# Kernel optimization log

Measured on AMD Instinct MI355X. Metric: run time of the kernel, lower is better.

Reference implementation:

```python
import jax, jax.numpy as jnp
import numpy as np
import math

B, S, C, H = 32, 500, 1024, 16
D = C // H  # head dim = 64

def setup_inputs() -> dict:
    key = jax.random.key(0)
    ks = jax.random.split(key, 9)
    sc = 1.0 / math.sqrt(C)
    return {
        "x": jax.random.normal(ks[0], (B, S, C), dtype=jnp.float32),
        "Wq": jax.random.normal(ks[1], (C, C), dtype=jnp.float32) * sc,
        "bq": jnp.zeros((C,), dtype=jnp.float32),
        "Wk": jax.random.normal(ks[2], (C, C), dtype=jnp.float32) * sc,
        "bk": jnp.zeros((C,), dtype=jnp.float32),
        "Wv": jax.random.normal(ks[3], (C, C), dtype=jnp.float32) * sc,
        "bv": jnp.zeros((C,), dtype=jnp.float32),
        "Wp": jax.random.normal(ks[4], (C, C), dtype=jnp.float32) * sc,
        "bp": jnp.zeros((C,), dtype=jnp.float32),
    }

def reference(x, Wq, bq, Wk, bk, Wv, bv, Wp, bp):
    # Projections -> [B, H, S, D]
    q = (x @ Wq + bq).reshape(B, S, H, D).transpose(0, 2, 1, 3)
    k = (x @ Wk + bk).reshape(B, S, H, D).transpose(0, 2, 1, 3)
    v = (x @ Wv + bv).reshape(B, S, H, D).transpose(0, 2, 1, 3)
    # Scaled scores [B, H, S, S]
    att = jnp.einsum('bhqd,bhkd->bhqk', q, k) * (1.0 / math.sqrt(D))
    causal = jnp.tril(jnp.ones((S, S), dtype=bool))
    att = jnp.where(causal[None, None], att, jnp.float32(-1e10))
    att = jax.nn.softmax(att, axis=-1)
    # (dropout is identity in eval mode)
    y = jnp.einsum('bhqk,bhkd->bhqd', att, v)  # [B, H, S, D]
    y = y.transpose(0, 2, 1, 3).reshape(B, S, C)
    return y @ Wp + bp
```

## Files before the change

### kernel.cpp

```cpp
#include <hip/hip_runtime.h>
#include <math.h>

#define B_ 32
#define S_ 500
#define C_ 1024
#define H_ 16
#define D_ 64
#define M_ (B_ * S_)
#define MP 16128
#define SP 512

typedef _Float16 f16;
typedef f16 f16x8 __attribute__((ext_vector_type(8)));
typedef f16 f16x4 __attribute__((ext_vector_type(4)));
typedef float f32x4 __attribute__((ext_vector_type(4)));

#define GLOBAL_AS __attribute__((address_space(1)))
#define LDS_AS __attribute__((address_space(3)))

__device__ __forceinline__ void async_load16(const void* g, void* l) {
    __builtin_amdgcn_global_load_lds((const GLOBAL_AS void*)g, (LDS_AS void*)l, 16, 0, 0);
}
template <int N>
__device__ __forceinline__ void wait_vmcnt() {
    asm volatile("s_waitcnt vmcnt(%0)" ::"i"(N) : "memory");
}

struct MaskF { static constexpr bool value = false; };
struct MaskT { static constexpr bool value = true; };

__global__ __launch_bounds__(256) void cast_rows(
    const float* __restrict__ in, f16* __restrict__ out, int n8_real, int n8_tot)
{
    int i = blockIdx.x * 256 + threadIdx.x;
    if (i >= n8_tot) return;
    f16x8 h;
    if (i < n8_real) {
        float4 a = ((const float4*)in)[2 * i];
        float4 b = ((const float4*)in)[2 * i + 1];
        h[0] = (f16)a.x; h[1] = (f16)a.y; h[2] = (f16)a.z; h[3] = (f16)a.w;
        h[4] = (f16)b.x; h[5] = (f16)b.y; h[6] = (f16)b.z; h[7] = (f16)b.w;
    } else {
        f16 z = (f16)0.f;
        h[0] = z; h[1] = z; h[2] = z; h[3] = z;
        h[4] = z; h[5] = z; h[6] = z; h[7] = z;
    }
    ((f16x8*)out)[i] = h;
}

__global__ __launch_bounds__(256) void castW_T4(
    const float* __restrict__ W0, const float* __restrict__ W1,
    const float* __restrict__ W2, const float* __restrict__ W3,
    f16* __restrict__ T0, f16* __restrict__ T1,
    f16* __restrict__ T2, f16* __restrict__ T3)
{
    __shared__ float t[32][33];
    const int z = blockIdx.z;
    const float* W = (z == 0) ? W0 : (z == 1) ? W1 : (z == 2) ? W2 : W3;
    f16* T = (z == 0) ? T0 : (z == 1) ? T1 : (z == 2) ? T2 : T3;
    const int n0 = blockIdx.x * 32, k0 = blockIdx.y * 32;
    const int tx = threadIdx.x, ty = threadIdx.y;
#pragma unroll
    for (int i = 0; i < 4; ++i)
        t[ty + 8 * i][tx] = W[(size_t)(k0 + ty + 8 * i) * C_ + n0 + tx];
    __syncthreads();
#pragma unroll
    for (int i = 0; i < 4; ++i) {
        int n = ty + 8 * i;
        T[(size_t)(n0 + n) * C_ + k0 + tx] = (f16)t[tx][n];
    }
}

#define BAR()                          \
    __builtin_amdgcn_s_barrier();      \
    __builtin_amdgcn_sched_barrier(0)

#define LD_A(MH)                                                              \
    _Pragma("unroll") for (int i = 0; i < 4; ++i)                             \
    _Pragma("unroll") for (int ks = 0; ks < 2; ++ks)                          \
        af[i][ks] = *(const f16x8*)(smem + c * 32768 + rowA +                 \
                                    ((MH) * 64 + i * 16) * 64 + sw[ks]);

#define LD_B(NH)                                                              \
    _Pragma("unroll") for (int j = 0; j < 2; ++j)                             \
    _Pragma("unroll") for (int ks = 0; ks < 2; ++ks)                          \
        bf[NH][j][ks] = *(const f16x8*)(smem + c * 32768 + rowB +             \
                                        ((NH) * 32 + j * 16) * 64 + sw[ks]);

#define MMA(MH, NH)                                                           \
    __builtin_amdgcn_s_setprio(1);                                            \
    _Pragma("unroll") for (int i = 0; i < 4; ++i)                             \
    _Pragma("unroll") for (int j = 0; j < 2; ++j)                             \
    _Pragma("unroll") for (int ks = 0; ks < 2; ++ks)                          \
        acc[(MH) * 4 + i][(NH) * 2 + j] =                                     \
            __builtin_amdgcn_mfma_f32_16x16x32_f16(                           \
                af[i][ks], bf[NH][j][ks], acc[(MH) * 4 + i][(NH) * 2 + j],    \
                0, 0, 0);                                                     \
    __builtin_amdgcn_s_setprio(0)

template <int MODE>
__global__ __launch_bounds__(512) void gemm256(
    const f16* __restrict__ A, const f16* __restrict__ W,
    const float* __restrict__ b0, const float* __restrict__ b1,
    const float* __restrict__ b2, void* __restrict__ o0,
    void* __restrict__ o1, void* __restrict__ o2)
{
    constexpr int K = C_;
    constexpr int NB = (MODE == 0) ? 12 : 4;
    constexpr int NWG = 63 * NB;
    constexpr int Q8 = NWG / 8, R8 = NWG % 8;
    extern __shared__ __align__(16) f16 smem[];

    const int tid = threadIdx.x;
    const int lane = tid & 63, w = tid >> 6;
    const int wm = w >> 2, wn = w & 3;
    const int quad = lane >> 4, lr = lane & 15;

    const int lin = blockIdx.x;
    const int xcd = lin & 7, pos = lin >> 3;
    const int wg = (xcd < R8 ? xcd * (Q8 + 1) : R8 * (Q8 + 1) + (xcd - R8) * Q8) + pos;
    const int m0 = (wg / NB) * 256;
    const int n0 = (wg % NB) * 256;

    const int srow = tid >> 3, sj = tid & 7;
    const int gc = sj ^ (srow & 7);
    const f16* pA = A + (size_t)(m0 + srow) * K + gc * 8;
    const f16* pB = W + (size_t)(n0 + srow) * K + gc * 8;
    f16* dA = smem + tid * 8;
    f16* dB = smem + 16384 + tid * 8;

    auto stageA = [&](int kt, int cb, int h) __attribute__((always_inline)) {
        const f16* s = pA + (size_t)(h * 128) * K + kt * 64;
        f16* d = dA + cb * 32768 + h * 8192;
        async_load16(s, d);
        async_load16(s + (size_t)64 * K, d + 4096);
    };
    auto stageB = [&](int kt, int cb, int h) __attribute__((always_inline)) {
        const f16* s = pB + (size_t)(h * 128) * K + kt * 64;
        f16* d = dB + cb * 32768 + h * 8192;
        async_load16(s, d);
        async_load16(s + (size_t)64 * K, d + 4096);
    };

    int sw[2];
    sw[0] = ((0 + quad) ^ (lr & 7)) * 8;
    sw[1] = ((4 + quad) ^ (lr & 7)) * 8;
    const int rowA = (wm * 128 + lr) * 64;
    const int rowB = 16384 + (wn * 64 + lr) * 64;

    f32x4 acc[8][4];
#pragma unroll
    for (int i = 0; i < 8; ++i)
#pragma unroll
        for (int j = 0; j < 4; ++j) acc[i][j] = (f32x4)0.f;
    f16x8 af[4][2], bf[2][2][2];

    stageA(0, 0, 0); stageA(0, 0, 1); stageB(0, 0, 0); stageB(0, 0, 1);

    constexpr int NT = K / 64;
    for (int kt = 0; kt < NT; ++kt) {
        const int c = kt & 1;
        BAR();
        if (kt + 1 < NT) {
            stageA(kt + 1, c ^ 1, 0); stageA(kt + 1, c ^ 1, 1);
            stageB(kt + 1, c ^ 1, 0); stageB(kt + 1, c ^ 1, 1);
            wait_vmcnt<8>();
        } else {
            wait_vmcnt<0>();
        }
        BAR();
        LD_A(0); LD_B(0);
        MMA(0, 0);
        LD_B(1);
        MMA(0, 1);
        LD_A(1);
        MMA(1, 1);
        MMA(1, 0);
    }

#pragma unroll
    for (int nf = 0; nf < 4; ++nf) {
        int gcn = n0 + wn * 64 + nf * 16 + lr;
        if (MODE == 1) {
            float bv = b0[gcn];
            float* of = (float*)o0;
#pragma unroll
            for (int mf = 0; mf < 8; ++mf) {
                int gr0 = m0 + wm * 128 + mf * 16 + quad * 4;
                if (gr0 >= M_) continue;
#pragma unroll
                for (int r = 0; r < 4; ++r)
                    of[(size_t)(gr0 + r) * C_ + gcn] = acc[mf][nf][r] + bv;
            }
        } else {
            int sec = gcn >> 10;
            int gcl = gcn & 1023;
            const float* bp = (sec == 0) ? b0 : (sec == 1) ? b1 : b2;
            float bv = bp[gcl];
            float osc = (sec == 0) ? 0.125f : 1.0f;
            int h = gcl >> 6, d = gcl & 63;
#pragma unroll
            for (int mf = 0; mf < 8; ++mf) {
                int gr0 = m0 + wm * 128 + mf * 16 + quad * 4;
                if (gr0 >= M_) continue;
                int b = gr0 / S_, s0 = gr0 - b * S_;
                if (sec < 2) {
                    f16* oq = (f16*)((sec == 0) ? o0 : o1);
#pragma unroll
                    for (int r = 0; r < 4; ++r) {
                        float v = (acc[mf][nf][r] + bv) * osc;
                        size_t idx = (((size_t)b * H_ + h) * S_ + (s0 + r)) * D_ + d;
                        oq[idx] = (f16)v;
                    }
                } else {
                    f16* ov = (f16*)o2;
                    f16x4 pk;
#pragma unroll
                    for (int r = 0; r < 4; ++r) pk[r] = (f16)(acc[mf][nf][r] + bv);
                    *(f16x4*)(ov + (((size_t)b * H_ + h) * D_ + d) * SP + s0) = pk;
                }
            }
        }
    }
}

__global__ __launch_bounds__(256) void attn_mfma(
    const f16* __restrict__ qg, const f16* __restrict__ kg,
    const f16* __restrict__ vt, f16* __restrict__ Y)
{
    __shared__ __align__(16) f16 sK[2][64 * 64];
    __shared__ __align__(16) f16 sVt[2][64 * 64];
    __shared__ __align__(16) f16 sP[4 * 32 * 64];

    const int tid = threadIdx.x;
    const int lin = blockIdx.x;
    const int xcd = lin & 7;
    const int pos = lin >> 3;
    const int bh = xcd * 64 + (pos >> 2);
    const int qt = 3 - (pos & 3);
    const int q0 = qt * 128;
    const int lane = tid & 63, w = tid >> 6;
    const int quad = lane >> 4, lr = lane & 15;
    const size_t gbase = (size_t)bh * S_ * D_;
    const size_t vbase = (size_t)bh * D_ * SP;
    const int psw = (lr & 7) << 1;

    f16x8 qf[2][2];
#pragma unroll
    for (int t = 0; t < 2; ++t) {
        int q = q0 + w * 32 + t * 16 + lr;
        const f16* pq = qg + gbase + (size_t)q * D_;
#pragma unroll
        for (int s2 = 0; s2 < 2; ++s2)
            qf[t][s2] = *(const f16x8*)(pq + quad * 8 + 32 * s2);
    }

    f32x4 accO[2][4];
#pragma unroll
    for (int t = 0; t < 2; ++t)
#pragma unroll
        for (int nt = 0; nt < 4; ++nt) accO[t][nt] = (f32x4)0.f;
    float l_run[2] = {0.f, 0.f};

    const int NT = 2 * qt + 2;

    auto stage = [&](int kt, int buf) __attribute__((always_inline)) {
        const int k0 = kt * 64;
#pragma unroll
        for (int it = 0; it < 2; ++it) {
            int idx = it * 256 + tid;
            int row = idx >> 3, c = idx & 7;
            int csw = (c ^ (row & 7)) * 8;
            async_load16(kg + gbase + (size_t)(k0 + row) * D_ + csw, &sK[buf][idx * 8]);
            async_load16(vt + vbase + (size_t)row * SP + k0 + csw, &sVt[buf][idx * 8]);
        }
    };

    auto step = [&](int kt, auto masked_tag) __attribute__((always_inline)) {
        constexpr bool MASKED = decltype(masked_tag)::value;
        const int cur = kt & 1;
        if (kt + 1 < NT) stage(kt + 1, cur ^ 1);
        const int k0 = kt * 64;

        f32x4 accS[4][2];
#pragma unroll
        for (int mt = 0; mt < 4; ++mt)
#pragma unroll
            for (int t = 0; t < 2; ++t) accS[mt][t] = (f32x4)0.f;
#pragma unroll
        for (int mt = 0; mt < 4; ++mt) {
            int row = mt * 16 + lr;
#pragma unroll
            for (int s2 = 0; s2 < 2; ++s2) {
                int off = row * 64 + (((quad + 4 * s2) ^ (lr & 7)) << 3);
                f16x8 ka = *(const f16x8*)&sK[cur][off];
#pragma unroll
                for (int t = 0; t < 2; ++t)
                    accS[mt][t] = __builtin_amdgcn_mfma_f32_16x16x32_f16(
                        ka, qf[t][s2], accS[mt][t], 0, 0, 0);
            }
        }

        float ls[2] = {0.f, 0.f};
#pragma unroll
        for (int mt = 0; mt < 4; ++mt)
#pragma unroll
            for (int t = 0; t < 2; ++t) {
                f16x4 pk;
#pragma unroll
                for (int r = 0; r < 4; ++r) {
                    float s = accS[mt][t][r];
                    if (MASKED) {
                        int key = k0 + mt * 16 + quad * 4 + r;
                        int qq = q0 + w * 32 + t * 16 + lr;
                        s = (key <= qq && key < S_) ? s : -1e30f;
                    }
                    float p = __expf(s);
                    ls[t] += p;
                    pk[r] = (f16)p;
                }
                int c8 = (mt * 4 + quad) ^ psw;
                *(f16x4*)&sP[w * 2048 + (t * 16 + lr) * 64 + c8 * 4] = pk;
            }
        ls[0] += __shfl_xor(ls[0], 16); ls[0] += __shfl_xor(ls[0], 32);
        ls[1] += __shfl_xor(ls[1], 16); ls[1] += __shfl_xor(ls[1], 32);
        l_run[0] += ls[0];
        l_run[1] += ls[1];

#pragma unroll
        for (int t = 0; t < 2; ++t) {
            int pb = w * 2048 + (t * 16 + lr) * 64;
#pragma unroll
            for (int s2 = 0; s2 < 2; ++s2) {
                int c8 = (quad * 2 + 8 * s2) ^ psw;
                f16x8 pf = *(const f16x8*)&sP[pb + c8 * 4];
#pragma unroll
                for (int nt = 0; nt < 4; ++nt) {
                    f16x8 vf = *(const f16x8*)
                        &sVt[cur][(nt * 16 + lr) * 64 + (((quad + 4 * s2) ^ (lr & 7)) << 3)];
                    accO[t][nt] = __builtin_amdgcn_mfma_f32_16x16x32_f16(
                        pf, vf, accO[t][nt], 0, 0, 0);
                }
            }
        }
        __syncthreads();
    };

    stage(0, 0);
    __syncthreads();
    for (int kt = 0; kt < 2 * qt; ++kt) step(kt, MaskF{});
    step(2 * qt, MaskT{});
    step(2 * qt + 1, MaskT{});

    const int b = bh >> 4, h = bh & 15;
#pragma unroll
    for (int t = 0; t < 2; ++t) {
#pragma unroll
        for (int r = 0; r < 4; ++r) {
            float lsum = __shfl(l_run[t], quad * 4 + r);
            float iv = 1.f / lsum;
            int s = q0 + w * 32 + t * 16 + quad * 4 + r;
            if (s >= S_) continue;
            size_t rowbase = (size_t)(b * S_ + s) * C_ + h * 64;
#pragma unroll
            for (int nt = 0; nt < 4; ++nt)
                Y[rowbase + nt * 16 + lr] = (f16)(accO[t][nt][r] * iv);
        }
    }
}

extern "C" void kernel_launch(void* const* d_in, const int* in_sizes, int n_in,
                              void* d_out, int out_size, void* d_ws, size_t ws_size,
                              hipStream_t stream)
{
    const float* x = (const float*)d_in[0];
    const float* Wq = (const float*)d_in[1];
    const float* bq = (const float*)d_in[2];
    const float* Wk = (const float*)d_in[3];
    const float* bk = (const float*)d_in[4];
    const float* Wv = (const float*)d_in[5];
    const float* bv = (const float*)d_in[6];
    const float* Wp = (const float*)d_in[7];
    const float* bp = (const float*)d_in[8];

    const size_t NEL = (size_t)M_ * C_;
    const size_t WEL = (size_t)C_ * C_;
    f16* qf = (f16*)d_ws;
    f16* kf = qf + NEL;
    f16* vtw = kf + NEL;
    f16* xf = vtw + (size_t)B_ * H_ * D_ * SP;
    f16* wpf = xf + (size_t)MP * C_;
    f16* yf = xf;

    f16* wq = (f16*)d_out;
    f16* wk = wq + WEL;
    f16* wv = wk + WEL;

    hipFuncSetAttribute(reinterpret_cast<const void*>(&gemm256<0>),
                        hipFuncAttributeMaxDynamicSharedMemorySize, 131072);
    hipFuncSetAttribute(reinterpret_cast<const void*>(&gemm256<1>),
                        hipFuncAttributeMaxDynamicSharedMemorySize, 131072);

    castW_T4<<<dim3(32, 32, 4), dim3(32, 8), 0, stream>>>(
        Wq, Wk, Wv, Wp, wq, wk, wv, wpf);

    int n8r = (int)(NEL / 8);
    int n8t = (int)((size_t)MP * C_ / 8);
    cast_rows<<<(n8t + 255) / 256, 256, 0, stream>>>(x, xf, n8r, n8t);

    gemm256<0><<<756, 512, 131072, stream>>>(xf, wq, bq, bk, bv, qf, kf, vtw);

    attn_mfma<<<2048, 256, 0, stream>>>(qf, kf, vtw, yf);

    gemm256<1><<<252, 512, 131072, stream>>>(yf, wpf, bp, nullptr, nullptr,
                                             d_out, nullptr, nullptr);
}
```

Before: 375.7 us.

## Read K and V fragments directly from global memory in attention, drop LDS staging

```diff
diff --git a/kernel.cpp b/kernel.cpp
--- a/kernel.cpp
+++ b/kernel.cpp
@@ -224,12 +224,10 @@
     }
 }
 
-__global__ __launch_bounds__(256) void attn_mfma(
+__global__ __launch_bounds__(256, 4) void attn_mfma(
     const f16* __restrict__ qg, const f16* __restrict__ kg,
     const f16* __restrict__ vt, f16* __restrict__ Y)
 {
-    __shared__ __align__(16) f16 sK[2][64 * 64];
-    __shared__ __align__(16) f16 sVt[2][64 * 64];
     __shared__ __align__(16) f16 sP[4 * 32 * 64];
 
     const int tid = threadIdx.x;
@@ -262,24 +260,8 @@
         for (int nt = 0; nt < 4; ++nt) accO[t][nt] = (f32x4)0.f;
     float l_run[2] = {0.f, 0.f};
 
-    const int NT = 2 * qt + 2;
-
-    auto stage = [&](int kt, int buf) __attribute__((always_inline)) {
-        const int k0 = kt * 64;
-#pragma unroll
-        for (int it = 0; it < 2; ++it) {
-            int idx = it * 256 + tid;
-            int row = idx >> 3, c = idx & 7;
-            int csw = (c ^ (row & 7)) * 8;
-            async_load16(kg + gbase + (size_t)(k0 + row) * D_ + csw, &sK[buf][idx * 8]);
-            async_load16(vt + vbase + (size_t)row * SP + k0 + csw, &sVt[buf][idx * 8]);
-        }
-    };
-
     auto step = [&](int kt, auto masked_tag) __attribute__((always_inline)) {
         constexpr bool MASKED = decltype(masked_tag)::value;
-        const int cur = kt & 1;
-        if (kt + 1 < NT) stage(kt + 1, cur ^ 1);
         const int k0 = kt * 64;
 
         f32x4 accS[4][2];
@@ -287,19 +269,20 @@
         for (int mt = 0; mt < 4; ++mt)
 #pragma unroll
             for (int t = 0; t < 2; ++t) accS[mt][t] = (f32x4)0.f;
+        __builtin_amdgcn_s_setprio(1);
 #pragma unroll
         for (int mt = 0; mt < 4; ++mt) {
-            int row = mt * 16 + lr;
+            const f16* pk_ = kg + gbase + (size_t)(k0 + mt * 16 + lr) * D_;
 #pragma unroll
             for (int s2 = 0; s2 < 2; ++s2) {
-                int off = row * 64 + (((quad + 4 * s2) ^ (lr & 7)) << 3);
-                f16x8 ka = *(const f16x8*)&sK[cur][off];
+                f16x8 ka = *(const f16x8*)(pk_ + quad * 8 + 32 * s2);
 #pragma unroll
                 for (int t = 0; t < 2; ++t)
                     accS[mt][t] = __builtin_amdgcn_mfma_f32_16x16x32_f16(
                         ka, qf[t][s2], accS[mt][t], 0, 0, 0);
             }
         }
+        __builtin_amdgcn_s_setprio(0);
 
         float ls[2] = {0.f, 0.f};
 #pragma unroll
@@ -327,6 +310,7 @@
         l_run[0] += ls[0];
         l_run[1] += ls[1];
 
+        __builtin_amdgcn_s_setprio(1);
 #pragma unroll
         for (int t = 0; t < 2; ++t) {
             int pb = w * 2048 + (t * 16 + lr) * 64;
@@ -336,18 +320,16 @@
                 f16x8 pf = *(const f16x8*)&sP[pb + c8 * 4];
 #pragma unroll
                 for (int nt = 0; nt < 4; ++nt) {
-                    f16x8 vf = *(const f16x8*)
-                        &sVt[cur][(nt * 16 + lr) * 64 + (((quad + 4 * s2) ^ (lr & 7)) << 3)];
+                    f16x8 vf = *(const f16x8*)(vt + vbase +
+                        (size_t)(nt * 16 + lr) * SP + k0 + quad * 8 + s2 * 32);
                     accO[t][nt] = __builtin_amdgcn_mfma_f32_16x16x32_f16(
                         pf, vf, accO[t][nt], 0, 0, 0);
                 }
             }
         }
-        __syncthreads();
+        __builtin_amdgcn_s_setprio(0);
     };
 
-    stage(0, 0);
-    __syncthreads();
     for (int kt = 0; kt < 2 * qt; ++kt) step(kt, MaskF{});
     step(2 * qt, MaskT{});
     step(2 * qt + 1, MaskT{});
```

Result: slower. 437.2 us (+16.4%).
